# Optimization experiments

Measured on AMD Instinct MI355X. Metric: run time of the kernel, lower is better.

The kernel has to match this reference:

```python
import jax, jax.numpy as jnp
import numpy as np

C, H, W = 1024, 128, 128

def setup_inputs() -> dict:
    key = jax.random.key(0)
    k1, k2 = jax.random.split(key)
    x = jax.random.normal(k1, (C, H, W), dtype=jnp.float32)
    gamma = jax.random.normal(k2, (1,), dtype=jnp.float32)
    return {"x": x, "gamma": gamma}

def reference(x, gamma):
    c, h, w = x.shape
    q = x.reshape(c, h * w)                      # (C, HW)
    energy = jnp.matmul(q, q.T)                  # (C, C)
    # negated-energy softmax: softmax(max(energy) - energy) along last dim
    energy_new = jnp.max(energy, axis=-1, keepdims=True) - energy
    attention = jax.nn.softmax(energy_new, axis=-1)
    out = jnp.matmul(attention, q).reshape(c, h, w)
    return gamma * out + x
```

## Files before the change

### kernel.cpp

```cpp
#include <hip/hip_runtime.h>
#include <hip/hip_bf16.h>

typedef unsigned short u16;
typedef float  f32x16 __attribute__((ext_vector_type(16)));
typedef short  bf16x8 __attribute__((ext_vector_type(8)));
typedef u16    u16x8  __attribute__((ext_vector_type(8)));

#define CDIM 1024
#define HW   16384

typedef const void __attribute__((address_space(1))) gvoid;
typedef void __attribute__((address_space(3))) svoid;

__device__ __forceinline__ u16 f2bf(float f) {
    unsigned u = __float_as_uint(f);
    u += 0x7fffu + ((u >> 16) & 1u);
    return (u16)(u >> 16);
}
__device__ __forceinline__ float bf2f(u16 h) { return __uint_as_float(((unsigned)h) << 16); }

__device__ __forceinline__ f32x16 mfma32(bf16x8 a, bf16x8 b, f32x16 c) {
    return __builtin_amdgcn_mfma_f32_32x32x16_bf16(a, b, c, 0, 0, 0);
}

__global__ __launch_bounds__(256) void k_convert(const float* __restrict__ x,
                                                 u16* __restrict__ hi, u16* __restrict__ lo,
                                                 u16* __restrict__ hiT)
{
    __shared__ u16 tile[64][72];
    const int pb = blockIdx.x;
    const int cb = blockIdx.y;
    const int tid = threadIdx.x;
#pragma unroll
    for (int pass = 0; pass < 4; ++pass) {
        const int i  = (tid >> 4) + (pass << 4);
        const int j4 = (tid & 15) << 2;
        const long gidx = (long)(cb * 64 + i) * HW + pb * 64 + j4;
        const float4 v = *(const float4*)(x + gidx);
        ushort4 h, l;
        h.x = f2bf(v.x); l.x = f2bf(v.x - bf2f(h.x));
        h.y = f2bf(v.y); l.y = f2bf(v.y - bf2f(h.y));
        h.z = f2bf(v.z); l.z = f2bf(v.z - bf2f(h.z));
        h.w = f2bf(v.w); l.w = f2bf(v.w - bf2f(h.w));
        *(ushort4*)(hi + gidx) = h;
        *(ushort4*)(lo + gidx) = l;
        tile[i][j4 + 0] = h.x; tile[i][j4 + 1] = h.y;
        tile[i][j4 + 2] = h.z; tile[i][j4 + 3] = h.w;
    }
    __syncthreads();
#pragma unroll
    for (int pass = 0; pass < 2; ++pass) {
        const int j  = (tid >> 3) + (pass << 5);
        const int c8 = (tid & 7) << 3;
        u16x8 v;
#pragma unroll
        for (int q = 0; q < 8; ++q) v[q] = tile[c8 + q][j];
        *(u16x8*)(hiT + (long)(pb * 64 + j) * CDIM + cb * 64 + c8) = v;
    }
}


__device__ __forceinline__ void stage_half(const u16* __restrict__ gbase, long ldg,
                                           int rowhalf, int ktile, u16* seg, int tid)
{
    const int wv = tid >> 6;
#pragma unroll
    for (int q = 0; q < 2; ++q) {
        const int lin16 = (q << 9) + tid;
        const int r    = lin16 >> 3;
        const int slot = lin16 & 7;
        const int gc   = (slot ^ (r & 7)) << 3;
        const u16* src = gbase + (long)((rowhalf << 7) + r) * ldg + (ktile << 6) + gc;
        u16* dst = seg + (q << 12) + (wv << 9);
        __builtin_amdgcn_global_load_lds((gvoid*)src, (svoid*)dst, 16, 0, 0);
    }
}

__device__ __forceinline__ bf16x8 rd_frag(const u16* seg, int row, int kk, int lane)
{
    const int c = (kk << 4) + ((lane >> 5) << 3);
    return *(const bf16x8*)(seg + row * 64 + (c ^ ((row & 7) << 3)));
}

#define SBAR()  do { __builtin_amdgcn_sched_barrier(0); \
                     __builtin_amdgcn_s_barrier();      \
                     __builtin_amdgcn_sched_barrier(0); } while (0)

template<int EPI>
__global__ __launch_bounds__(512, 2) void k_gemm8(
    const u16* __restrict__ Amat, const u16* __restrict__ Bhi, const u16* __restrict__ Blo,
    long lda, long ldb, int kchunk, int nbn,
    float* __restrict__ C, long ldc, long csplit,
    const float* __restrict__ X, const float* __restrict__ gamma)
{
    __shared__ u16 sA[2][2][8192];
    __shared__ u16 sB[2][2][8192];

    const int tid  = threadIdx.x;
    const int lane = tid & 63;
    const int w    = tid >> 6;
    const int wm   = w >> 2;
    const int wn   = w & 3;
    const int l31  = lane & 31;

    const int ks   = blockIdx.y;
    const int nblk = gridDim.x;
    const int lin  = blockIdx.x;
    const int ti   = (lin & 7) * (nblk >> 3) + (lin >> 3);
    const int bi   = ti / nbn, bn = ti % nbn;

    const u16* Ab = Amat + (long)bi * 256 * lda + (long)ks * kchunk;
    const u16* Bb;
    if (EPI == 0) {
        const int half = nbn >> 1;
        Bb = (bn < half) ? (Bhi + (long)bn * 256 * ldb)
                         : (Blo + (long)(bn - half) * 256 * ldb);
    } else {
        Bb = Bhi + (long)bn * 256 * ldb;
    }
    Bb += (long)ks * kchunk;

    const int nkt = kchunk >> 6;

    f32x16 acc[4][2];
    {
        f32x16 z;
#pragma unroll
        for (int r = 0; r < 16; ++r) z[r] = 0.f;
#pragma unroll
        for (int f = 0; f < 4; ++f)
#pragma unroll
            for (int g = 0; g < 2; ++g) acc[f][g] = z;
    }

    stage_half(Ab, lda, 0, 0, sA[0][0], tid);
    stage_half(Bb, ldb, 1, 0, sB[0][1], tid);
    stage_half(Bb, ldb, 0, 0, sB[0][0], tid);
    stage_half(Ab, lda, 1, 0, sA[0][1], tid);
    if (nkt > 1) {
        stage_half(Ab, lda, 0, 1, sA[1][0], tid);
        stage_half(Bb, ldb, 1, 1, sB[1][1], tid);
    }

    bf16x8 Af[2][4], B0f[4], B1f[4];

    for (int u = 0; u < nkt; ++u) {
        const int db = u & 1;

        if (u >= nkt - 2) {
            asm volatile("s_waitcnt vmcnt(0)" ::: "memory");
            if (u + 1 < nkt) stage_half(Bb, ldb, 0, u + 1, sB[db ^ 1][0], tid);
        } else {
            stage_half(Bb, ldb, 0, u + 1, sB[db ^ 1][0], tid);
            asm volatile("s_waitcnt vmcnt(6)" ::: "memory");
        }
        SBAR();
#pragma unroll
        for (int f = 0; f < 2; ++f)
#pragma unroll
            for (int kk = 0; kk < 4; ++kk)
                Af[f][kk] = rd_frag(sA[db][0], wm * 64 + f * 32 + l31, kk, lane);
#pragma unroll
        for (int kk = 0; kk < 4; ++kk)
            B0f[kk] = rd_frag(sB[db][0], wn * 32 + l31, kk, lane);
        __builtin_amdgcn_s_setprio(1);
#pragma unroll
        for (int kk = 0; kk < 4; ++kk) {
            acc[0][0] = mfma32(Af[0][kk], B0f[kk], acc[0][0]);
            acc[1][0] = mfma32(Af[1][kk], B0f[kk], acc[1][0]);
        }
        __builtin_amdgcn_s_setprio(0);
        SBAR();

        if (u + 1 < nkt) stage_half(Ab, lda, 1, u + 1, sA[db ^ 1][1], tid);
#pragma unroll
        for (int kk = 0; kk < 4; ++kk)
            B1f[kk] = rd_frag(sB[db][1], wn * 32 + l31, kk, lane);
        __builtin_amdgcn_s_setprio(1);
#pragma unroll
        for (int kk = 0; kk < 4; ++kk) {
            acc[0][1] = mfma32(Af[0][kk], B1f[kk], acc[0][1]);
            acc[1][1] = mfma32(Af[1][kk], B1f[kk], acc[1][1]);
        }
        __builtin_amdgcn_s_setprio(0);
        SBAR();

        if (u + 2 < nkt) stage_half(Ab, lda, 0, u + 2, sA[db][0], tid);
#pragma unroll
        for (int f = 0; f < 2; ++f)
#pragma unroll
            for (int kk = 0; kk < 4; ++kk)
                Af[f][kk] = rd_frag(sA[db][1], wm * 64 + f * 32 + l31, kk, lane);
        __builtin_amdgcn_s_setprio(1);
#pragma unroll
        for (int kk = 0; kk < 4; ++kk) {
            acc[2][1] = mfma32(Af[0][kk], B1f[kk], acc[2][1]);
            acc[3][1] = mfma32(Af[1][kk], B1f[kk], acc[3][1]);
        }
        __builtin_amdgcn_s_setprio(0);
        SBAR();

        if (u + 2 < nkt) stage_half(Bb, ldb, 1, u + 2, sB[db][1], tid);
        __builtin_amdgcn_s_setprio(1);
#pragma unroll
        for (int kk = 0; kk < 4; ++kk) {
            acc[2][0] = mfma32(Af[0][kk], B0f[kk], acc[2][0]);
            acc[3][0] = mfma32(Af[1][kk], B0f[kk], acc[3][0]);
        }
        __builtin_amdgcn_s_setprio(0);
        SBAR();
    }

    if (EPI == 0) {
        float* Cb = C + (long)ks * csplit;
#pragma unroll
        for (int f = 0; f < 4; ++f)
#pragma unroll
            for (int g = 0; g < 2; ++g)
#pragma unroll
                for (int r = 0; r < 16; ++r) {
                    const int row = bi * 256 + (f >> 1) * 128 + wm * 64 + (f & 1) * 32
                                    + (r & 3) + ((r >> 2) << 3) + ((lane >> 5) << 2);
                    const int col = bn * 256 + g * 128 + wn * 32 + l31;
                    Cb[(long)row * ldc + col] = acc[f][g][r];
                }
    } else {
        const float gm = gamma[0];
#pragma unroll
        for (int f = 0; f < 4; ++f)
#pragma unroll
            for (int g = 0; g < 2; ++g)
#pragma unroll
                for (int r = 0; r < 16; ++r) {
                    const int row = bi * 256 + (f >> 1) * 128 + wm * 64 + (f & 1) * 32
                                    + (r & 3) + ((r >> 2) << 3) + ((lane >> 5) << 2);
                    const int col = bn * 256 + g * 128 + wn * 32 + l31;
                    const long idx = (long)row * ldc + col;
                    C[idx] = gm * acc[f][g][r] + X[idx];
                }
    }
}

__global__ __launch_bounds__(256) void k_symmetrize(const float* __restrict__ E12,
                                                    float* __restrict__ Esym)
{
    __shared__ float tr[64][65];
    const int jb = blockIdx.x, ib = blockIdx.y, tid = threadIdx.x;
    float4 accv[4];
#pragma unroll
    for (int e4 = 0; e4 < 4; ++e4) {
        const int e = tid + (e4 << 8);
        const int i = e >> 4, j4 = (e & 15) << 2;
        float ax = 0, ay = 0, az = 0, aw = 0, bx = 0, by = 0, bz = 0, bw = 0;
#pragma unroll
        for (int ks = 0; ks < 8; ++ks) {
            const float* base = E12 + (long)ks * (1024 * 2048);
            float4 p1 = *(const float4*)(base + (long)(ib * 64 + i) * 2048 + jb * 64 + j4);
            float4 p2 = *(const float4*)(base + (long)(ib * 64 + i) * 2048 + 1024 + jb * 64 + j4);
            float4 p3 = *(const float4*)(base + (long)(jb * 64 + i) * 2048 + 1024 + ib * 64 + j4);
            ax += p1.x + p2.x; ay += p1.y + p2.y; az += p1.z + p2.z; aw += p1.w + p2.w;
            bx += p3.x; by += p3.y; bz += p3.z; bw += p3.w;
        }
        accv[e4] = make_float4(ax, ay, az, aw);
        tr[i][j4 + 0] = bx; tr[i][j4 + 1] = by; tr[i][j4 + 2] = bz; tr[i][j4 + 3] = bw;
    }
    __syncthreads();
#pragma unroll
    for (int e4 = 0; e4 < 4; ++e4) {
        const int e = tid + (e4 << 8);
        const int i = e >> 4, j4 = (e & 15) << 2;
        float4 o = accv[e4];
        o.x += tr[j4 + 0][i]; o.y += tr[j4 + 1][i]; o.z += tr[j4 + 2][i]; o.w += tr[j4 + 3][i];
        *(float4*)(Esym + (long)(ib * 64 + i) * CDIM + jb * 64 + j4) = o;
    }
}

__global__ __launch_bounds__(256) void k_softmax(const float* __restrict__ E, u16* __restrict__ att)
{
    __shared__ float red[4];
    __shared__ float bcast;
    const int row = blockIdx.x, tid = threadIdx.x;
    const float4 v = ((const float4*)(E + (long)row * CDIM))[tid];

    float m = fminf(fminf(v.x, v.y), fminf(v.z, v.w));
#pragma unroll
    for (int s = 32; s > 0; s >>= 1) m = fminf(m, __shfl_down(m, s));
    if ((tid & 63) == 0) red[tid >> 6] = m;
    __syncthreads();
    if (tid == 0) bcast = fminf(fminf(red[0], red[1]), fminf(red[2], red[3]));
    __syncthreads();
    m = bcast;

    const float px = expf(m - v.x), py = expf(m - v.y), pz = expf(m - v.z), pw = expf(m - v.w);
    float s4 = px + py + pz + pw;
#pragma unroll
    for (int s = 32; s > 0; s >>= 1) s4 += __shfl_down(s4, s);
    if ((tid & 63) == 0) red[tid >> 6] = s4;
    __syncthreads();
    if (tid == 0) bcast = red[0] + red[1] + red[2] + red[3];
    __syncthreads();
    const float inv = 1.0f / bcast;

    ushort4 o;
    o.x = f2bf(px * inv); o.y = f2bf(py * inv); o.z = f2bf(pz * inv); o.w = f2bf(pw * inv);
    ((ushort4*)(att + (long)row * CDIM))[tid] = o;
}

extern "C" void kernel_launch(void* const* d_in, const int* in_sizes, int n_in,
                              void* d_out, int out_size, void* d_ws, size_t ws_size,
                              hipStream_t stream)
{
    (void)in_sizes; (void)n_in; (void)out_size; (void)ws_size;
    const float* x = (const float*)d_in[0];
    const float* gamma = (const float*)d_in[1];
    float* out = (float*)d_out;
    char* ws = (char*)d_ws;

    u16*   hi   = (u16*)ws;
    u16*   lo   = (u16*)(ws + (32ull << 20));
    u16*   hiT  = (u16*)(ws + (64ull << 20));
    float* Esym = (float*)(ws + (96ull << 20));
    u16*   att  = (u16*)(ws + (100ull << 20));
    float* E12  = out;

    k_convert<<<dim3(256, 16), 256, 0, stream>>>(x, hi, lo, hiT);
    k_gemm8<0><<<dim3(32, 8), 512, 0, stream>>>(hi, hi, lo, (long)HW, (long)HW, 2048, 8,
                                                E12, 2048L, 1024L * 2048L, nullptr, nullptr);
    k_symmetrize<<<dim3(16, 16), 256, 0, stream>>>(E12, Esym);
    k_softmax<<<1024, 256, 0, stream>>>(Esym, att);
    k_gemm8<1><<<dim3(256, 1), 512, 0, stream>>>(att, hiT, nullptr, 1024L, 1024L, 1024, 64,
                                                 out, (long)HW, 0L, x, gamma);
}
```

Baseline: 189.6 us.

## Simplify GEMM pipeline to one barrier per k-tile and remap LDS swizzle

Replaces the four-phase, staggered half-tile prefetch schedule (four barriers per k-tile) with a plain double-buffer loop. Each iteration issues all four half-tile loads for the next k-tile, waits for the current tile, and does all 32 MFMAs between a single barrier. It also changes the LDS layout so each wave writes 8-row blocks with an XOR swizzle keyed on the row within the block, and updates the fragment reads to match. The intent is less synchronization overhead and simpler address math, at the cost of shallower load/compute interleaving and more fragment registers live at once.

```diff
diff --git a/kernel.cpp b/kernel.cpp
--- a/kernel.cpp
+++ b/kernel.cpp
@@ -59,27 +59,28 @@
     }
 }
 
-
 __device__ __forceinline__ void stage_half(const u16* __restrict__ gbase, long ldg,
                                            int rowhalf, int ktile, u16* seg, int tid)
 {
-    const int wv = tid >> 6;
+    const int lane = tid & 63;
+    const int wv   = tid >> 6;
+    const int s    = lane >> 3;
+    const int r7   = (lane & 7) ^ s;
+    const int col  = s << 3;
 #pragma unroll
     for (int q = 0; q < 2; ++q) {
-        const int lin16 = (q << 9) + tid;
-        const int r    = lin16 >> 3;
-        const int slot = lin16 & 7;
-        const int gc   = (slot ^ (r & 7)) << 3;
-        const u16* src = gbase + (long)((rowhalf << 7) + r) * ldg + (ktile << 6) + gc;
-        u16* dst = seg + (q << 12) + (wv << 9);
-        __builtin_amdgcn_global_load_lds((gvoid*)src, (svoid*)dst, 16, 0, 0);
+        const int j = wv + (q << 3);
+        const u16* src = gbase + (long)((rowhalf << 7) + (j << 3) + r7) * ldg
+                               + (ktile << 6) + col;
+        __builtin_amdgcn_global_load_lds((gvoid*)src, (svoid*)(seg + (j << 9)), 16, 0, 0);
     }
 }
 
 __device__ __forceinline__ bf16x8 rd_frag(const u16* seg, int row, int kk, int lane)
 {
-    const int c = (kk << 4) + ((lane >> 5) << 3);
-    return *(const bf16x8*)(seg + row * 64 + (c ^ ((row & 7) << 3)));
+    const int s = (kk << 1) + (lane >> 5);
+    const int off = ((row >> 3) << 9) + (s << 6) + (((row & 7) ^ s) << 3);
+    return *(const bf16x8*)(seg + off);
 }
 
 #define SBAR()  do { __builtin_amdgcn_sched_barrier(0); \
@@ -134,81 +135,68 @@
     }
 
     stage_half(Ab, lda, 0, 0, sA[0][0], tid);
+    stage_half(Ab, lda, 1, 0, sA[0][1], tid);
+    stage_half(Bb, ldb, 0, 0, sB[0][0], tid);
     stage_half(Bb, ldb, 1, 0, sB[0][1], tid);
-    stage_half(Bb, ldb, 0, 0, sB[0][0], tid);
-    stage_half(Ab, lda, 1, 0, sA[0][1], tid);
-    if (nkt > 1) {
-        stage_half(Ab, lda, 0, 1, sA[1][0], tid);
-        stage_half(Bb, ldb, 1, 1, sB[1][1], tid);
-    }
-
-    bf16x8 Af[2][4], B0f[4], B1f[4];
 
     for (int u = 0; u < nkt; ++u) {
         const int db = u & 1;
 
-        if (u >= nkt - 2) {
+        SBAR();
+
+        if (u + 1 < nkt) {
+            stage_half(Ab, lda, 0, u + 1, sA[db ^ 1][0], tid);
+            stage_half(Ab, lda, 1, u + 1, sA[db ^ 1][1], tid);
+            stage_half(Bb, ldb, 0, u + 1, sB[db ^ 1][0], tid);
+            stage_half(Bb, ldb, 1, u + 1, sB[db ^ 1][1], tid);
+            asm volatile("s_waitcnt vmcnt(8)" ::: "memory");
+        } else {
             asm volatile("s_waitcnt vmcnt(0)" ::: "memory");
-            if (u + 1 < nkt) stage_half(Bb, ldb, 0, u + 1, sB[db ^ 1][0], tid);
-        } else {
-            stage_half(Bb, ldb, 0, u + 1, sB[db ^ 1][0], tid);
-            asm volatile("s_waitcnt vmcnt(6)" ::: "memory");
-        }
-        SBAR();
+        }
+
+        bf16x8 A0f[2][4], B0f[4], B1f[4];
 #pragma unroll
         for (int f = 0; f < 2; ++f)
 #pragma unroll
             for (int kk = 0; kk < 4; ++kk)
-                Af[f][kk] = rd_frag(sA[db][0], wm * 64 + f * 32 + l31, kk, lane);
-#pragma unroll
-        for (int kk = 0; kk < 4; ++kk)
-            B0f[kk] = rd_frag(sB[db][0], wn * 32 + l31, kk, lane);
+                A0f[f][kk] = rd_frag(sA[db][0], wm * 64 + f * 32 + l31, kk, lane);
+#pragma unroll
+        for (int kk = 0; kk < 4; ++kk) B0f[kk] = rd_frag(sB[db][0], wn * 32 + l31, kk, lane);
+#pragma unroll
+        for (int kk = 0; kk < 4; ++kk) B1f[kk] = rd_frag(sB[db][1], wn * 32 + l31, kk, lane);
+
         __builtin_amdgcn_s_setprio(1);
 #pragma unroll
         for (int kk = 0; kk < 4; ++kk) {
-            acc[0][0] = mfma32(Af[0][kk], B0f[kk], acc[0][0]);
-            acc[1][0] = mfma32(Af[1][kk], B0f[kk], acc[1][0]);
+            acc[0][0] = mfma32(A0f[0][kk], B0f[kk], acc[0][0]);
+            acc[1][0] = mfma32(A0f[1][kk], B0f[kk], acc[1][0]);
+        }
+#pragma unroll
+        for (int kk = 0; kk < 4; ++kk) {
+            acc[0][1] = mfma32(A0f[0][kk], B1f[kk], acc[0][1]);
+            acc[1][1] = mfma32(A0f[1][kk], B1f[kk], acc[1][1]);
         }
         __builtin_amdgcn_s_setprio(0);
-        SBAR();
-
-        if (u + 1 < nkt) stage_half(Ab, lda, 1, u + 1, sA[db ^ 1][1], tid);
-#pragma unroll
-        for (int kk = 0; kk < 4; ++kk)
-            B1f[kk] = rd_frag(sB[db][1], wn * 32 + l31, kk, lane);
+
+        bf16x8 A1f[2][4];
+#pragma unroll
+        for (int f = 0; f < 2; ++f)
+#pragma unroll
+            for (int kk = 0; kk < 4; ++kk)
+                A1f[f][kk] = rd_frag(sA[db][1], wm * 64 + f * 32 + l31, kk, lane);
+
         __builtin_amdgcn_s_setprio(1);
 #pragma unroll
         for (int kk = 0; kk < 4; ++kk) {
-            acc[0][1] = mfma32(Af[0][kk], B1f[kk], acc[0][1]);
-            acc[1][1] = mfma32(Af[1][kk], B1f[kk], acc[1][1]);
+            acc[2][1] = mfma32(A1f[0][kk], B1f[kk], acc[2][1]);
+            acc[3][1] = mfma32(A1f[1][kk], B1f[kk], acc[3][1]);
+        }
+#pragma unroll
+        for (int kk = 0; kk < 4; ++kk) {
+            acc[2][0] = mfma32(A1f[0][kk], B0f[kk], acc[2][0]);
+            acc[3][0] = mfma32(A1f[1][kk], B0f[kk], acc[3][0]);
         }
         __builtin_amdgcn_s_setprio(0);
-        SBAR();
-
-        if (u + 2 < nkt) stage_half(Ab, lda, 0, u + 2, sA[db][0], tid);
-#pragma unroll
-        for (int f = 0; f < 2; ++f)
-#pragma unroll
-            for (int kk = 0; kk < 4; ++kk)
-                Af[f][kk] = rd_frag(sA[db][1], wm * 64 + f * 32 + l31, kk, lane);
-        __builtin_amdgcn_s_setprio(1);
-#pragma unroll
-        for (int kk = 0; kk < 4; ++kk) {
-            acc[2][1] = mfma32(Af[0][kk], B1f[kk], acc[2][1]);
-            acc[3][1] = mfma32(Af[1][kk], B1f[kk], acc[3][1]);
-        }
-        __builtin_amdgcn_s_setprio(0);
-        SBAR();
-
-        if (u + 2 < nkt) stage_half(Bb, ldb, 1, u + 2, sB[db][1], tid);
-        __builtin_amdgcn_s_setprio(1);
-#pragma unroll
-        for (int kk = 0; kk < 4; ++kk) {
-            acc[2][0] = mfma32(Af[0][kk], B0f[kk], acc[2][0]);
-            acc[3][0] = mfma32(Af[1][kk], B0f[kk], acc[3][0]);
-        }
-        __builtin_amdgcn_s_setprio(0);
-        SBAR();
     }
 
     if (EPI == 0) {
```

After: 208.0 us. 1.1x slower.
